# Performance work log

Measured on AMD Instinct MI355X. Metric: run time of the kernel, lower is better.

The kernel has to match this reference:

```python
import jax, jax.numpy as jnp
import numpy as np

D, T, B = 128, 64, 512
EPS = 1e-5


def setup_inputs() -> dict:
    key = jax.random.key(0)
    k1, k2, k3, k4, k5 = jax.random.split(key, 5)
    inp = jax.random.normal(k1, (D, T, B), jnp.float32) * 0.1
    returns_partition = jax.random.normal(k2, (D, T, B), jnp.float32) * 0.01
    target = jax.random.normal(k3, (D,), jnp.float32) * 0.1
    hidden = jnp.zeros((D, 1, B), jnp.float32)  # forward arg (overwritten at t=0)
    # diagonally-dominant weight so the per-row denominators v[j,j] stay away from 0
    W = jnp.eye(D, dtype=jnp.float32) + 0.1 * jax.random.normal(k4, (D, D), jnp.float32)
    b = 0.1 * jax.random.normal(k5, (D,), jnp.float32)
    return {"input": inp, "target": target, "returns_partition": returns_partition,
            "hidden": hidden, "W": W, "b": b}


def _recurrence(h, v, absb, pi_bar):
    # h, pi_bar: [D, B]; v: [D, D] (row-normalized); absb: [D]
    d = h.shape[0]
    vd = jnp.diagonal(v)                                  # v[j, j], torch.matmul(vj, e_j)
    s = v @ (h - pi_bar)                                  # [D, B], s[j] = vj . (h - pi_bar)
    lam_p = (absb[:, None] - s) / vd[:, None]
    lam_m = (-absb[:, None] - s) / vd[:, None]
    delta = (jnp.where(s > absb[:, None], lam_p, 0.0)
             + jnp.where(s < -absb[:, None], lam_m, 0.0))  # [D, B]
    # hidden_new_j = h + delta[j] * e_j  =>  v @ (hidden_new_j - pi_bar) = s + v[:, j] (x) delta[j]
    snew = s[None, :, :] + v.T[:, :, None] * delta[:, None, :]      # [J, D, B]
    inside = (snew < absb[None, :, None] + EPS) & (snew > -absb[None, :, None] - EPS)
    # torch: judge_mat[j] = min over rows; then max over j  == any_j(all_k(...))
    judge_mat = jnp.any(jnp.all(inside, axis=1), axis=0).astype(h.dtype)  # [B]

    # sequential per-coordinate projection (order matters: row j uses updated state)
    def body(ht, j):
        sj = v[j] @ (ht - pi_bar)                          # [B]
        lp = (absb[j] - sj) / v[j, j]
        lm = (-absb[j] - sj) / v[j, j]
        dj = jnp.where(sj > absb[j], lp, 0.0) + jnp.where(sj < -absb[j], lm, 0.0)
        return ht.at[j].add(dj), None
    h_temp, _ = jax.lax.scan(body, h, jnp.arange(d))

    # 10-step bisection between pi_bar (feasible) and (1 - judge_mat) * h
    def bis(carry, _):
        h_in, h_out = carry
        h_m = h_in + (h_out - h_in) * 0.5
        sm = v @ (h_m - pi_bar)
        j = jnp.all((sm <= absb[:, None] + EPS) & (sm >= -absb[:, None] - EPS), axis=0)  # [B]
        return (jnp.where(j, h_m, h_in), jnp.where(j, h_out, h_m)), h_m
    h_out0 = (1.0 - judge_mat) * h
    _, h_ms = jax.lax.scan(bis, (pi_bar, h_out0), None, length=10)
    h_m = h_ms[-1]
    return judge_mat * h_temp + (1.0 - judge_mat) * h_m


def reference(input, target, returns_partition, hidden, W, b):
    d, t, bsz = input.shape
    norm = jnp.linalg.norm(W, axis=1, keepdims=True)
    v = W / jnp.maximum(norm, 1e-12)                      # F.normalize(W, p=2, dim=1)
    absb = jnp.abs(b)
    pi_bar = jnp.broadcast_to(target[:, None], (d, bsz))  # [D, B]

    h0 = input[:, 0, :]                                   # t = 0: hidden := input slice
    rs = jnp.moveaxis(returns_partition[:, :t - 1, :], 1, 0)  # [T-1, D, B]

    def step(h, r):
        adj = h * (1.0 + r) / (1.0 + jnp.sum(h * r, axis=0))
        hn = _recurrence(adj, v, absb, pi_bar)
        return hn, hn

    h_last, hs = jax.lax.scan(step, h0, rs)
    output = jnp.concatenate([h0[:, None, :], jnp.moveaxis(hs, 0, 1)], axis=1)  # [D, T, B]
    return output, h_last[:, None, :]
```

## Files before the change

kernel.cpp:

```cpp
#include <hip/hip_runtime.h>
#include <cstdint>

#define D 128
#define T 64
#define B 512
#define EPSF 1e-5f

__device__ __forceinline__ float lane_bcast(float x, int l) {
    return __int_as_float(__builtin_amdgcn_readlane(__float_as_int(x), l));
}

__global__ __launch_bounds__(64) void prep_kernel(const float* __restrict__ W,
                                                  const float* __restrict__ b,
                                                  float* __restrict__ vT,
                                                  float* __restrict__ vd,
                                                  float* __restrict__ absb) {
    const int i = blockIdx.x;
    const int l = threadIdx.x;
    float w0 = W[i * D + l];
    float w1 = W[i * D + l + 64];
    float p = w0 * w0 + w1 * w1;
#pragma unroll
    for (int off = 32; off; off >>= 1) p += __shfl_xor(p, off);
    float norm = sqrtf(p);
    float scale = norm > 1e-12f ? norm : 1e-12f;
    float v0 = w0 / scale;
    float v1 = w1 / scale;
    vT[l * D + i] = v0;
    vT[(l + 64) * D + i] = v1;
    if (i < 64) {
        if (l == i) vd[i] = v0;
    } else {
        if (l == i - 64) vd[i] = v1;
    }
    if (i == 0) {
        absb[l] = fabsf(b[l]);
        absb[l + 64] = fabsf(b[l + 64]);
    }
}

__global__ __launch_bounds__(128) void rnn_kernel(const float* __restrict__ input,
                                                  const float* __restrict__ target,
                                                  const float* __restrict__ returns,
                                                  const float* __restrict__ vTg,
                                                  const float* __restrict__ vdg,
                                                  const float* __restrict__ absbg,
                                                  float* __restrict__ out) {
    __shared__ float vsh[D * D];

    const int tid = threadIdx.x;
    {
        const float4* src = (const float4*)vTg;
        float4* dst = (float4*)vsh;
#pragma unroll
        for (int c = 0; c < 32; ++c) {
            int f = c * 128 + tid;
            int k = f >> 5;
            int i = (f & 31) << 2;
            int ck = (k & 7) << 2;
            int d4 = k * 32 + (((i ^ ck)) >> 2);
            dst[d4] = src[f];
        }
    }
    __syncthreads();

    const int w = tid >> 6;
    const int lane = tid & 63;
    const int b = blockIdx.x * 2 + w;
    const int rlo = lane, rhi = lane + 64;

    const float tgt_lo = target[rlo], tgt_hi = target[rhi];
    const float a_lo = absbg[rlo], a_hi = absbg[rhi];
    const float aeps_lo = a_lo + EPSF, aeps_hi = a_hi + EPSF;
    const float vd_lo = vdg[rlo], vd_hi = vdg[rhi];
    const float rvd_lo = 1.0f / vd_lo, rvd_hi = 1.0f / vd_hi;

    int ax[8];
#pragma unroll
    for (int c = 0; c < 8; ++c) ax[c] = rlo ^ (c << 2);

    const int cj = (lane & 7) << 2;
    int Abase[8];
#pragma unroll
    for (int c = 0; c < 8; ++c) Abase[c] = lane * 128 + ((c << 2) ^ cj);

    float h_lo = input[rlo * T * B + b];
    float h_hi = input[rhi * T * B + b];
    out[rlo * T * B + b] = h_lo;
    out[rhi * T * B + b] = h_hi;

    float r_lo = returns[rlo * T * B + b];
    float r_hi = returns[rhi * T * B + b];

    for (int t = 1; t < T; ++t) {
        float num_lo = h_lo * (1.0f + r_lo);
        float num_hi = h_hi * (1.0f + r_hi);
        float p = h_lo * r_lo + h_hi * r_hi;
#pragma unroll
        for (int off = 32; off; off >>= 1) p += __shfl_xor(p, off);
        float den = 1.0f + p;
        float adj_lo = num_lo / den;
        float adj_hi = num_hi / den;

        if (t < T - 1) {
            r_lo = returns[rlo * T * B + t * B + b];
            r_hi = returns[rhi * T * B + t * B + b];
        }

        const float x_lo = adj_lo - tgt_lo;
        const float x_hi = adj_hi - tgt_hi;

        float s_lo = 0.0f, s_hi = 0.0f;
#pragma unroll
        for (int k = 0; k < 64; ++k) {
            float xb = lane_bcast(x_lo, k);
            s_lo = fmaf(vsh[k * 128 + ax[k & 7]], xb, s_lo);
            s_hi = fmaf(vsh[k * 128 + ax[k & 7] + 64], xb, s_hi);
        }
#pragma unroll
        for (int k = 0; k < 64; ++k) {
            float xb = lane_bcast(x_hi, k);
            s_lo = fmaf(vsh[(k + 64) * 128 + ax[k & 7]], xb, s_lo);
            s_hi = fmaf(vsh[(k + 64) * 128 + ax[k & 7] + 64], xb, s_hi);
        }

        h_lo = adj_lo;
        h_hi = adj_hi;

        bool viol_lo = (s_lo > a_lo) || (s_lo < -a_lo);
        bool viol_hi = (s_hi > a_hi) || (s_hi < -a_hi);
        uint64_t mlo = __ballot(viol_lo);
        uint64_t mhi = __ballot(viol_hi);

        if ((mlo | mhi) != 0ull) {
            float dl = 0.0f, dh = 0.0f;
            if (s_lo > a_lo) dl = (a_lo - s_lo) / vd_lo;
            else if (s_lo < -a_lo) dl = (-a_lo - s_lo) / vd_lo;
            if (s_hi > a_hi) dh = (a_hi - s_hi) / vd_hi;
            else if (s_hi < -a_hi) dh = (-a_hi - s_hi) / vd_hi;

            int V = __popcll(mlo) + __popcll(mhi);
            bool judge;

            if (V <= 8) {
                bool in_lo = (s_lo < aeps_lo) && (s_lo > -aeps_lo);
                bool in_hi = (s_hi < aeps_hi) && (s_hi > -aeps_hi);
                judge = (__ballot(in_lo && in_hi) == ~0ull);
                if (!judge) {
                    uint64_t t_mlo = mlo, t_mhi = mhi;
                    while (t_mlo | t_mhi) {
                        int j;
                        float dj;
                        if (t_mlo) {
                            int jl = (int)__ffsll((unsigned long long)t_mlo) - 1;
                            t_mlo &= t_mlo - 1;
                            j = jl;
                            dj = lane_bcast(dl, jl);
                        } else {
                            int jh = (int)__ffsll((unsigned long long)t_mhi) - 1;
                            t_mhi &= t_mhi - 1;
                            j = 64 + jh;
                            dj = lane_bcast(dh, jh);
                        }
                        int cjj = (j & 7) << 2;
                        int base = j * 128 + (rlo ^ cjj);
                        float n_lo = fmaf(vsh[base], dj, s_lo);
                        float n_hi = fmaf(vsh[base + 64], dj, s_hi);
                        bool pl = (n_lo < aeps_lo) && (n_lo > -aeps_lo);
                        bool ph = (n_hi < aeps_hi) && (n_hi > -aeps_hi);
                        if (__ballot(pl && ph) == ~0ull) { judge = true; break; }
                    }
                }
            } else {
                float m1 = -1.0f, m2 = -1.0f;
#pragma unroll
                for (int a = 0; a < 4; ++a) {
#pragma unroll
                    for (int c = 0; c < 8; ++c) {
                        const int i0 = a * 32 + c * 4;
                        const float* p1 = &vsh[Abase[c] + 32 * a];
                        float4 c1 = *(const float4*)p1;
                        float4 c2 = *(const float4*)(p1 + 8192);
#pragma unroll
                        for (int e = 0; e < 4; ++e) {
                            const int i = i0 + e;
                            float sv = (i < 64) ? lane_bcast(s_lo, i)
                                                : lane_bcast(s_hi, i - 64);
                            float ae = (i < 64) ? lane_bcast(aeps_lo, i)
                                                : lane_bcast(aeps_hi, i - 64);
                            float f1 = ((const float*)&c1)[e];
                            float f2 = ((const float*)&c2)[e];
                            m1 = fmaxf(m1, fabsf(fmaf(f1, dl, sv)) - ae);
                            m2 = fmaxf(m2, fabsf(fmaf(f2, dh, sv)) - ae);
                        }
                    }
                }
                judge = ((__ballot(m1 < 0.0f) | __ballot(m2 < 0.0f)) != 0ull);
            }

            if (judge) {
                uint64_t rem_lo = ~0ull, rem_hi = ~0ull;
                while (true) {
                    uint64_t m1b = __ballot((s_lo > a_lo) || (s_lo < -a_lo)) & rem_lo;
                    uint64_t m2b = __ballot((s_hi > a_hi) || (s_hi < -a_hi)) & rem_hi;
                    int j;
                    if (m1b) {
                        int jl = (int)__ffsll((unsigned long long)m1b) - 1;
                        j = jl;
                        rem_lo = (jl == 63) ? 0ull : (~0ull << (jl + 1));
                    } else if (m2b) {
                        int jh = (int)__ffsll((unsigned long long)m2b) - 1;
                        j = 64 + jh;
                        rem_lo = 0ull;
                        rem_hi = (jh == 63) ? 0ull : (~0ull << (jh + 1));
                    } else {
                        break;
                    }
                    float dl2 = (s_lo > a_lo) ? (a_lo - s_lo) * rvd_lo
                               : ((s_lo < -a_lo) ? (-a_lo - s_lo) * rvd_lo : 0.0f);
                    float dh2 = (s_hi > a_hi) ? (a_hi - s_hi) * rvd_hi
                               : ((s_hi < -a_hi) ? (-a_hi - s_hi) * rvd_hi : 0.0f);
                    float srcv = (j < 64) ? dl2 : dh2;
                    float dj = lane_bcast(srcv, j & 63);
                    if (lane == (j & 63)) {
                        if (j < 64) h_lo += dj; else h_hi += dj;
                    }
                    int cjj = (j & 7) << 2;
                    int base = j * 128 + (rlo ^ cjj);
                    s_lo = fmaf(vsh[base], dj, s_lo);
                    s_hi = fmaf(vsh[base + 64], dj, s_hi);
                }
            } else {
                float hin_lo = tgt_lo, hin_hi = tgt_hi;
                float sin_lo = 0.0f, sin_hi = 0.0f;
                float hout_lo = h_lo, hout_hi = h_hi;
                float sout_lo = s_lo, sout_hi = s_hi;
                float hm_lo = 0.0f, hm_hi = 0.0f;
#pragma unroll
                for (int it = 0; it < 10; ++it) {
                    hm_lo = hin_lo + (hout_lo - hin_lo) * 0.5f;
                    hm_hi = hin_hi + (hout_hi - hin_hi) * 0.5f;
                    float sm_lo = sin_lo + (sout_lo - sin_lo) * 0.5f;
                    float sm_hi = sin_hi + (sout_hi - sin_hi) * 0.5f;
                    bool pl = (sm_lo <= aeps_lo) && (sm_lo >= -aeps_lo);
                    bool ph = (sm_hi <= aeps_hi) && (sm_hi >= -aeps_hi);
                    bool inside = (__ballot(pl && ph) == ~0ull);
                    if (inside) {
                        hin_lo = hm_lo; hin_hi = hm_hi;
                        sin_lo = sm_lo; sin_hi = sm_hi;
                    } else {
                        hout_lo = hm_lo; hout_hi = hm_hi;
                        sout_lo = sm_lo; sout_hi = sm_hi;
                    }
                }
                h_lo = hm_lo;
                h_hi = hm_hi;
            }
        }

        out[rlo * T * B + t * B + b] = h_lo;
        out[rhi * T * B + t * B + b] = h_hi;
    }

    out[D * T * B + rlo * B + b] = h_lo;
    out[D * T * B + rhi * B + b] = h_hi;
}

extern "C" void kernel_launch(void* const* d_in, const int* in_sizes, int n_in,
                              void* d_out, int out_size, void* d_ws, size_t ws_size,
                              hipStream_t stream) {
    const float* input   = (const float*)d_in[0];
    const float* target  = (const float*)d_in[1];
    const float* returns = (const float*)d_in[2];
    const float* W = (const float*)d_in[4];
    const float* b = (const float*)d_in[5];
    float* out = (float*)d_out;

    float* vT   = (float*)d_ws;
    float* vd   = vT + D * D;
    float* absb = vd + D;

    prep_kernel<<<D, 64, 0, stream>>>(W, b, vT, vd, absb);
    rnn_kernel<<<B / 2, 128, 0, stream>>>(input, target, returns, vT, vd, absb, out);
}
```

Baseline: 216.8 us.

## Share V rows across two waves via LDS for the matvec, pair-pack columns

The per-step matvec used to run inside each wave as 128 readlane broadcasts, with every wave reading all of V. Now each thread owns one row of V, stored row-major and swizzled. It computes dot products against both waves' x vectors, which are staged in LDS, and the two waves swap halves of the result through shared memory. A second copy of V is laid out as float2 pairs for the column accesses in the projection and judge loops. This reuses each V load for two batch elements and uses vector LDS reads, at the cost of two block-wide barriers per timestep and double the LDS footprint.

```diff
diff --git a/kernel.cpp b/kernel.cpp
--- a/kernel.cpp
+++ b/kernel.cpp
@@ -46,28 +46,46 @@
                                                   const float* __restrict__ vdg,
                                                   const float* __restrict__ absbg,
                                                   float* __restrict__ out) {
-    __shared__ float vsh[D * D];
+    __shared__ __align__(16) float  vrow[D * D];
+    __shared__ __align__(16) float2 vpair[D * 64];
+    __shared__ __align__(16) float  xsh[2][D];
+    __shared__ float ssh[2][64];
 
     const int tid = threadIdx.x;
-    {
-        const float4* src = (const float4*)vTg;
-        float4* dst = (float4*)vsh;
-#pragma unroll
-        for (int c = 0; c < 32; ++c) {
-            int f = c * 128 + tid;
-            int k = f >> 5;
-            int i = (f & 31) << 2;
-            int ck = (k & 7) << 2;
-            int d4 = k * 32 + (((i ^ ck)) >> 2);
-            dst[d4] = src[f];
-        }
+    const int lane = tid & 63;
+    const int wid = tid >> 6;
+
+#pragma unroll
+    for (int c = 0; c < 32; ++c) {
+        int f = c * 128 + tid;
+        int k = f >> 5;
+        int i0 = (f & 31) << 1;
+        float4 val;
+        val.x = vTg[k * D + i0];
+        val.y = vTg[k * D + i0 + 64];
+        val.z = vTg[k * D + i0 + 1];
+        val.w = vTg[k * D + i0 + 65];
+        *(float4*)&vpair[(k << 6) + (i0 ^ ((k & 3) << 2))] = val;
+    }
+#pragma unroll
+    for (int c = 0; c < 32; ++c) {
+        int f = c * 128 + tid;
+        int i = f >> 5;
+        int k0 = (f & 31) << 2;
+        float4 val;
+        val.x = vTg[k0 * D + i];
+        val.y = vTg[(k0 + 1) * D + i];
+        val.z = vTg[(k0 + 2) * D + i];
+        val.w = vTg[(k0 + 3) * D + i];
+        *(float4*)&vrow[i * D + (k0 ^ ((i & 7) << 2))] = val;
     }
     __syncthreads();
 
-    const int w = tid >> 6;
-    const int lane = tid & 63;
-    const int b = blockIdx.x * 2 + w;
+    const int b = blockIdx.x * 2 + wid;
     const int rlo = lane, rhi = lane + 64;
+    const int mrow = wid * 64 + lane;
+    const float* vr = &vrow[mrow * D];
+    const int swr = (mrow & 7) << 2;
 
     const float tgt_lo = target[rlo], tgt_hi = target[rhi];
     const float a_lo = absbg[rlo], a_hi = absbg[rhi];
@@ -75,15 +93,6 @@
     const float vd_lo = vdg[rlo], vd_hi = vdg[rhi];
     const float rvd_lo = 1.0f / vd_lo, rvd_hi = 1.0f / vd_hi;
 
-    int ax[8];
-#pragma unroll
-    for (int c = 0; c < 8; ++c) ax[c] = rlo ^ (c << 2);
-
-    const int cj = (lane & 7) << 2;
-    int Abase[8];
-#pragma unroll
-    for (int c = 0; c < 8; ++c) Abase[c] = lane * 128 + ((c << 2) ^ cj);
-
     float h_lo = input[rlo * T * B + b];
     float h_hi = input[rhi * T * B + b];
     out[rlo * T * B + b] = h_lo;
@@ -107,25 +116,37 @@
             r_hi = returns[rhi * T * B + t * B + b];
         }
 
-        const float x_lo = adj_lo - tgt_lo;
-        const float x_hi = adj_hi - tgt_hi;
-
-        float s_lo = 0.0f, s_hi = 0.0f;
-#pragma unroll
-        for (int k = 0; k < 64; ++k) {
-            float xb = lane_bcast(x_lo, k);
-            s_lo = fmaf(vsh[k * 128 + ax[k & 7]], xb, s_lo);
-            s_hi = fmaf(vsh[k * 128 + ax[k & 7] + 64], xb, s_hi);
-        }
-#pragma unroll
-        for (int k = 0; k < 64; ++k) {
-            float xb = lane_bcast(x_hi, k);
-            s_lo = fmaf(vsh[(k + 64) * 128 + ax[k & 7]], xb, s_lo);
-            s_hi = fmaf(vsh[(k + 64) * 128 + ax[k & 7] + 64], xb, s_hi);
-        }
-
+        float x_lo = adj_lo - tgt_lo;
+        float x_hi = adj_hi - tgt_hi;
+        xsh[wid][rlo] = x_lo;
+        xsh[wid][rhi] = x_hi;
         h_lo = adj_lo;
         h_hi = adj_hi;
+
+        __syncthreads();
+
+        float s0 = 0.0f, s1 = 0.0f;
+#pragma unroll
+        for (int k4 = 0; k4 < D; k4 += 4) {
+            float4 vv = *(const float4*)&vr[k4 ^ swr];
+            float4 x0 = *(const float4*)&xsh[0][k4];
+            float4 x1 = *(const float4*)&xsh[1][k4];
+            s0 = fmaf(vv.x, x0.x, s0);
+            s0 = fmaf(vv.y, x0.y, s0);
+            s0 = fmaf(vv.z, x0.z, s0);
+            s0 = fmaf(vv.w, x0.w, s0);
+            s1 = fmaf(vv.x, x1.x, s1);
+            s1 = fmaf(vv.y, x1.y, s1);
+            s1 = fmaf(vv.z, x1.z, s1);
+            s1 = fmaf(vv.w, x1.w, s1);
+        }
+        ssh[wid ^ 1][lane] = wid ? s0 : s1;
+
+        __syncthreads();
+
+        float miss = ssh[wid][lane];
+        float s_lo = wid ? miss : s0;
+        float s_hi = wid ? s1 : miss;
 
         bool viol_lo = (s_lo > a_lo) || (s_lo < -a_lo);
         bool viol_hi = (s_hi > a_hi) || (s_hi < -a_hi);
@@ -162,54 +183,54 @@
                             j = 64 + jh;
                             dj = lane_bcast(dh, jh);
                         }
-                        int cjj = (j & 7) << 2;
-                        int base = j * 128 + (rlo ^ cjj);
-                        float n_lo = fmaf(vsh[base], dj, s_lo);
-                        float n_hi = fmaf(vsh[base + 64], dj, s_hi);
+                        float2 vj = vpair[(j << 6) + (lane ^ ((j & 3) << 2))];
+                        float n_lo = fmaf(vj.x, dj, s_lo);
+                        float n_hi = fmaf(vj.y, dj, s_hi);
                         bool pl = (n_lo < aeps_lo) && (n_lo > -aeps_lo);
                         bool ph = (n_hi < aeps_hi) && (n_hi > -aeps_hi);
                         if (__ballot(pl && ph) == ~0ull) { judge = true; break; }
                     }
                 }
             } else {
-                float m1 = -1.0f, m2 = -1.0f;
-#pragma unroll
-                for (int a = 0; a < 4; ++a) {
-#pragma unroll
-                    for (int c = 0; c < 8; ++c) {
-                        const int i0 = a * 32 + c * 4;
-                        const float* p1 = &vsh[Abase[c] + 32 * a];
-                        float4 c1 = *(const float4*)p1;
-                        float4 c2 = *(const float4*)(p1 + 8192);
-#pragma unroll
-                        for (int e = 0; e < 4; ++e) {
-                            const int i = i0 + e;
-                            float sv = (i < 64) ? lane_bcast(s_lo, i)
-                                                : lane_bcast(s_hi, i - 64);
-                            float ae = (i < 64) ? lane_bcast(aeps_lo, i)
-                                                : lane_bcast(aeps_hi, i - 64);
-                            float f1 = ((const float*)&c1)[e];
-                            float f2 = ((const float*)&c2)[e];
-                            m1 = fmaxf(m1, fabsf(fmaf(f1, dl, sv)) - ae);
-                            m2 = fmaxf(m2, fabsf(fmaf(f2, dh, sv)) - ae);
-                        }
-                    }
+                float m1a = -1.0f, m1b = -1.0f, m2a = -1.0f, m2b = -1.0f;
+                const float2* r1 = vpair + (lane << 6);
+                const float2* r2 = vpair + ((lane + 64) << 6);
+                const int swj = (lane & 3) << 2;
+#pragma unroll
+                for (int ii = 0; ii < 64; ii += 2) {
+                    const int ix = ii ^ swj;
+                    float4 c1 = *(const float4*)(r1 + ix);
+                    float4 c2 = *(const float4*)(r2 + ix);
+                    float sl0 = lane_bcast(s_lo, ii), sh0 = lane_bcast(s_hi, ii);
+                    float sl1 = lane_bcast(s_lo, ii + 1), sh1 = lane_bcast(s_hi, ii + 1);
+                    float al0 = lane_bcast(aeps_lo, ii), ah0 = lane_bcast(aeps_hi, ii);
+                    float al1 = lane_bcast(aeps_lo, ii + 1), ah1 = lane_bcast(aeps_hi, ii + 1);
+                    m1a = fmaxf(m1a, fabsf(fmaf(c1.x, dl, sl0)) - al0);
+                    m1b = fmaxf(m1b, fabsf(fmaf(c1.y, dl, sh0)) - ah0);
+                    m1a = fmaxf(m1a, fabsf(fmaf(c1.z, dl, sl1)) - al1);
+                    m1b = fmaxf(m1b, fabsf(fmaf(c1.w, dl, sh1)) - ah1);
+                    m2a = fmaxf(m2a, fabsf(fmaf(c2.x, dh, sl0)) - al0);
+                    m2b = fmaxf(m2b, fabsf(fmaf(c2.y, dh, sh0)) - ah0);
+                    m2a = fmaxf(m2a, fabsf(fmaf(c2.z, dh, sl1)) - al1);
+                    m2b = fmaxf(m2b, fabsf(fmaf(c2.w, dh, sh1)) - ah1);
                 }
+                float m1 = fmaxf(m1a, m1b);
+                float m2 = fmaxf(m2a, m2b);
                 judge = ((__ballot(m1 < 0.0f) | __ballot(m2 < 0.0f)) != 0ull);
             }
 
             if (judge) {
                 uint64_t rem_lo = ~0ull, rem_hi = ~0ull;
                 while (true) {
-                    uint64_t m1b = __ballot((s_lo > a_lo) || (s_lo < -a_lo)) & rem_lo;
-                    uint64_t m2b = __ballot((s_hi > a_hi) || (s_hi < -a_hi)) & rem_hi;
+                    uint64_t m1b_ = __ballot((s_lo > a_lo) || (s_lo < -a_lo)) & rem_lo;
+                    uint64_t m2b_ = __ballot((s_hi > a_hi) || (s_hi < -a_hi)) & rem_hi;
                     int j;
-                    if (m1b) {
-                        int jl = (int)__ffsll((unsigned long long)m1b) - 1;
+                    if (m1b_) {
+                        int jl = (int)__ffsll((unsigned long long)m1b_) - 1;
                         j = jl;
                         rem_lo = (jl == 63) ? 0ull : (~0ull << (jl + 1));
-                    } else if (m2b) {
-                        int jh = (int)__ffsll((unsigned long long)m2b) - 1;
+                    } else if (m2b_) {
+                        int jh = (int)__ffsll((unsigned long long)m2b_) - 1;
                         j = 64 + jh;
                         rem_lo = 0ull;
                         rem_hi = (jh == 63) ? 0ull : (~0ull << (jh + 1));
@@ -225,10 +246,9 @@
                     if (lane == (j & 63)) {
                         if (j < 64) h_lo += dj; else h_hi += dj;
                     }
-                    int cjj = (j & 7) << 2;
-                    int base = j * 128 + (rlo ^ cjj);
-                    s_lo = fmaf(vsh[base], dj, s_lo);
-                    s_hi = fmaf(vsh[base + 64], dj, s_hi);
+                    float2 vj = vpair[(j << 6) + (lane ^ ((j & 3) << 2))];
+                    s_lo = fmaf(vj.x, dj, s_lo);
+                    s_hi = fmaf(vj.y, dj, s_hi);
                 }
             } else {
                 float hin_lo = tgt_lo, hin_hi = tgt_hi;
```

New measurement: 278.4 us. 1.28x slower.
